# Optimization experiments

Hardware: AMD Instinct MI355X
Metric: run time of the kernel (lower is better)

## Reference

```python
import jax, jax.numpy as jnp
import numpy as np

EPS = 1e-8


def setup_inputs() -> dict:
    key = jax.random.key(0)
    k1, k2, k3 = jax.random.split(key, 3)
    T, B, d, n = 1024, 8, 64, 64
    v = jax.random.normal(k1, (T, B, d), dtype=jnp.float32)
    k = jax.random.normal(k2, (T, B, n), dtype=jnp.float32)
    alpha = jax.random.uniform(k3, (T, B, n), dtype=jnp.float32)
    return {"v": v, "k": k, "alpha": alpha}


def reference(v, k, alpha):
    # v: (T,B,d), k: (T,B,n), alpha: (T,B,n) in [0,1] -> S: (T,B,d,n)
    outer = jnp.einsum('tbd,tbn->tbdn', v, k)          # (T,B,d,n)
    log_alpha = jnp.log(jnp.maximum(alpha, EPS))       # clamp_min(1e-8)
    cumprod = jnp.exp(jnp.cumsum(log_alpha, axis=0))   # (T,B,n)
    decay = cumprod / (cumprod[-1:] + EPS)             # normalize by last step
    weighted = outer * decay[:, :, None, :]            # (T,B,d,n)
    S = jnp.cumsum(weighted, axis=0)
    return S
```

## Files before the change

### kernel.cpp

```cpp
#include <hip/hip_runtime.h>

#define T_DIM 1024
#define B_DIM 8
#define D_DIM 64
#define N_DIM 64

typedef float v4f __attribute__((ext_vector_type(4)));

#define WS_W 0
#define WS_PSUM 524288

template <int C>
__global__ __launch_bounds__(1024) void decay_w_kernel(
    const float* __restrict__ alpha, const float* __restrict__ kk,
    float* __restrict__ ws) {
  constexpr int LEN = T_DIM / C;
  constexpr int CPT = C / 16;
  const int b = blockIdx.x;
  const int tid = threadIdx.x;
  const int n = tid & 63;
  const int ci = tid >> 6;

  __shared__ float ls[C][N_DIM];

#pragma unroll
  for (int cc = 0; cc < CPT; ++cc) {
    const int c = cc * 16 + ci;
    float s = 0.f;
#pragma unroll 8
    for (int i = 0; i < LEN; ++i) {
      const int t = c * LEN + i;
      s += logf(fmaxf(alpha[((size_t)t * B_DIM + b) * N_DIM + n], 1e-8f));
    }
    ls[c][n] = s;
  }
  __syncthreads();

#pragma unroll
  for (int cc = 0; cc < CPT; ++cc) {
    const int c = cc * 16 + ci;
    float pre = 0.f, tot = 0.f;
#pragma unroll
    for (int j = 0; j < C; ++j) {
      const float sv = ls[j][n];
      tot += sv;
      if (j < c) pre += sv;
    }
    const float invden = 1.0f / (expf(tot) + 1e-8f);
    float cum = pre;
#pragma unroll 4
    for (int i = 0; i < LEN; ++i) {
      const size_t idx = ((size_t)(c * LEN + i) * B_DIM + b) * N_DIM + n;
      cum += logf(fmaxf(alpha[idx], 1e-8f));
      ws[WS_W + idx] = kk[idx] * expf(cum) * invden;
    }
  }
}

template <int C>
__global__ __launch_bounds__(256) void chunk_psum_kernel(
    const float* __restrict__ v, float* __restrict__ ws) {
  constexpr int LEN = T_DIM / C;
  const int bid = blockIdx.x;
  const int dt = bid & 3;
  const int b  = (bid >> 2) & 7;
  const int c  = bid >> 5;
  const int tid = threadIdx.x;
  const int d  = dt * 16 + (tid >> 4);
  const int n0 = (tid & 15) * 4;

  const float* __restrict__ vp = v + (size_t)b * D_DIM + d;
  const float* __restrict__ wp = ws + WS_W + (size_t)b * N_DIM + n0;

  v4f acc = {0.f, 0.f, 0.f, 0.f};
#pragma unroll 8
  for (int i = 0; i < LEN; ++i) {
    const int t = c * LEN + i;
    const float vv = vp[(size_t)t * (B_DIM * D_DIM)];
    const v4f w4 = *(const v4f*)(wp + (size_t)t * (B_DIM * N_DIM));
    acc.x = fmaf(vv, w4.x, acc.x);
    acc.y = fmaf(vv, w4.y, acc.y);
    acc.z = fmaf(vv, w4.z, acc.z);
    acc.w = fmaf(vv, w4.w, acc.w);
  }
  *(v4f*)(ws + WS_PSUM + (((size_t)c * B_DIM + b) * D_DIM + d) * N_DIM + n0) = acc;
}

template <int C>
__global__ __launch_bounds__(256) void scan_store_kernel(
    const float* __restrict__ v, const float* __restrict__ ws,
    float* __restrict__ out) {
  constexpr int LEN = T_DIM / C;
  const int bid = blockIdx.x;
  const int dt = bid & 3;
  const int b  = (bid >> 2) & 7;
  const int c  = bid >> 5;
  const int tid = threadIdx.x;
  const int d  = dt * 16 + (tid >> 4);
  const int n0 = (tid & 15) * 4;

  const float* __restrict__ vp = v + (size_t)b * D_DIM + d;
  const float* __restrict__ wp = ws + WS_W + (size_t)b * N_DIM + n0;
  const float* __restrict__ pp = ws + WS_PSUM + ((size_t)b * D_DIM + d) * N_DIM + n0;

  v4f acc = {0.f, 0.f, 0.f, 0.f};
#pragma unroll 4
  for (int j = 0; j < c; ++j) {
    const v4f p = *(const v4f*)(pp + (size_t)j * (B_DIM * D_DIM * N_DIM));
    acc.x += p.x; acc.y += p.y; acc.z += p.z; acc.w += p.w;
  }

#pragma unroll 8
  for (int i = 0; i < LEN; ++i) {
    const int t = c * LEN + i;
    const float vv = vp[(size_t)t * (B_DIM * D_DIM)];
    const v4f w4 = *(const v4f*)(wp + (size_t)t * (B_DIM * N_DIM));
    acc.x = fmaf(vv, w4.x, acc.x);
    acc.y = fmaf(vv, w4.y, acc.y);
    acc.z = fmaf(vv, w4.z, acc.z);
    acc.w = fmaf(vv, w4.w, acc.w);
    __builtin_nontemporal_store(
        acc, (v4f*)(out + (((size_t)t * B_DIM + b) * D_DIM + d) * N_DIM + n0));
  }
}

extern "C" void kernel_launch(void* const* d_in, const int* in_sizes, int n_in,
                              void* d_out, int out_size, void* d_ws, size_t ws_size,
                              hipStream_t stream) {
  const float* v     = (const float*)d_in[0];
  const float* k     = (const float*)d_in[1];
  const float* alpha = (const float*)d_in[2];
  float* out = (float*)d_out;
  float* ws  = (float*)d_ws;

  const size_t needed32 = (size_t)(WS_PSUM + 32 * B_DIM * D_DIM * N_DIM) * sizeof(float);
  if (ws_size >= needed32) {
    decay_w_kernel<32><<<B_DIM, 1024, 0, stream>>>(alpha, k, ws);
    chunk_psum_kernel<32><<<32 * 32, 256, 0, stream>>>(v, ws);
    scan_store_kernel<32><<<32 * 32, 256, 0, stream>>>(v, ws, out);
  } else {
    decay_w_kernel<16><<<B_DIM, 1024, 0, stream>>>(alpha, k, ws);
    chunk_psum_kernel<16><<<16 * 32, 256, 0, stream>>>(v, ws);
    scan_store_kernel<16><<<16 * 32, 256, 0, stream>>>(v, ws, out);
  }
}
```

Measured before the change: 183.1 us.

## Split decay into parallel chunk kernels, add psum prefix kernel, raise chunks to 64

Replaces the single-block-per-batch decay kernel with two kernels over 64 chunks per batch, so the log/exp decay work is spread across 512 blocks instead of 8. Adds a separate prefix-sum kernel over per-chunk partial sums so scan_store reads one precomputed prefix instead of looping over all previous chunks. Raises the chunk count to 64 when the workspace allows, fully unrolls the inner loops, and switches output stores from nontemporal to regular. The cost is two extra launches, more workspace traffic for the prefix buffer, and the risk that regular stores pollute cache.

```diff
diff --git a/kernel.cpp b/kernel.cpp
--- a/kernel.cpp
+++ b/kernel.cpp
@@ -7,53 +7,53 @@
 
 typedef float v4f __attribute__((ext_vector_type(4)));
 
+#define DC_CHUNKS 64
+#define DC_LEN 16
+
+#define SLAB (B_DIM * D_DIM * N_DIM)
+
 #define WS_W 0
-#define WS_PSUM 524288
+#define WS_PSUM (T_DIM * B_DIM * N_DIM)
 
-template <int C>
-__global__ __launch_bounds__(1024) void decay_w_kernel(
+__global__ __launch_bounds__(64) void decay_chunksum_kernel(
+    const float* __restrict__ alpha, float* __restrict__ lsum) {
+  const int b = blockIdx.x >> 6;
+  const int c = blockIdx.x & 63;
+  const int n = threadIdx.x;
+
+  float s = 0.f;
+#pragma unroll
+  for (int i = 0; i < DC_LEN; ++i) {
+    const int t = c * DC_LEN + i;
+    s += logf(fmaxf(alpha[((size_t)t * B_DIM + b) * N_DIM + n], 1e-8f));
+  }
+  lsum[((size_t)b * DC_CHUNKS + c) * N_DIM + n] = s;
+}
+
+__global__ __launch_bounds__(64) void decay_w_kernel(
     const float* __restrict__ alpha, const float* __restrict__ kk,
-    float* __restrict__ ws) {
-  constexpr int LEN = T_DIM / C;
-  constexpr int CPT = C / 16;
-  const int b = blockIdx.x;
-  const int tid = threadIdx.x;
-  const int n = tid & 63;
-  const int ci = tid >> 6;
+    const float* __restrict__ lsum, float* __restrict__ w) {
+  const int b = blockIdx.x >> 6;
+  const int c = blockIdx.x & 63;
+  const int n = threadIdx.x;
 
-  __shared__ float ls[C][N_DIM];
+  const float* __restrict__ lp = lsum + (size_t)b * DC_CHUNKS * N_DIM + n;
+  float pre = 0.f, tot = 0.f;
+#pragma unroll 8
+  for (int j = 0; j < DC_CHUNKS; ++j) {
+    const float sj = lp[(size_t)j * N_DIM];
+    pre += (j < c) ? sj : 0.f;
+    tot += sj;
+  }
+  const float invden = 1.0f / (expf(tot) + 1e-8f);
 
+  float cum = pre;
 #pragma unroll
-  for (int cc = 0; cc < CPT; ++cc) {
-    const int c = cc * 16 + ci;
-    float s = 0.f;
-#pragma unroll 8
-    for (int i = 0; i < LEN; ++i) {
-      const int t = c * LEN + i;
-      s += logf(fmaxf(alpha[((size_t)t * B_DIM + b) * N_DIM + n], 1e-8f));
-    }
-    ls[c][n] = s;
-  }
-  __syncthreads();
-
-#pragma unroll
-  for (int cc = 0; cc < CPT; ++cc) {
-    const int c = cc * 16 + ci;
-    float pre = 0.f, tot = 0.f;
-#pragma unroll
-    for (int j = 0; j < C; ++j) {
-      const float sv = ls[j][n];
-      tot += sv;
-      if (j < c) pre += sv;
-    }
-    const float invden = 1.0f / (expf(tot) + 1e-8f);
-    float cum = pre;
-#pragma unroll 4
-    for (int i = 0; i < LEN; ++i) {
-      const size_t idx = ((size_t)(c * LEN + i) * B_DIM + b) * N_DIM + n;
-      cum += logf(fmaxf(alpha[idx], 1e-8f));
-      ws[WS_W + idx] = kk[idx] * expf(cum) * invden;
-    }
+  for (int i = 0; i < DC_LEN; ++i) {
+    const int t = c * DC_LEN + i;
+    const size_t idx = ((size_t)t * B_DIM + b) * N_DIM + n;
+    cum += logf(fmaxf(alpha[idx], 1e-8f));
+    w[idx] = kk[idx] * expf(cum) * invden;
   }
 }
 
@@ -73,7 +73,7 @@
   const float* __restrict__ wp = ws + WS_W + (size_t)b * N_DIM + n0;
 
   v4f acc = {0.f, 0.f, 0.f, 0.f};
-#pragma unroll 8
+#pragma unroll
   for (int i = 0; i < LEN; ++i) {
     const int t = c * LEN + i;
     const float vv = vp[(size_t)t * (B_DIM * D_DIM)];
@@ -84,6 +84,21 @@
     acc.w = fmaf(vv, w4.w, acc.w);
   }
   *(v4f*)(ws + WS_PSUM + (((size_t)c * B_DIM + b) * D_DIM + d) * N_DIM + n0) = acc;
+}
+
+template <int C>
+__global__ __launch_bounds__(256) void psum_prefix_kernel(float* __restrict__ ws) {
+  const int q = blockIdx.x * 256 + threadIdx.x;
+  v4f* __restrict__ ps  = (v4f*)(ws + WS_PSUM);
+  v4f* __restrict__ pxs = ps + (size_t)C * (SLAB / 4);
+
+  v4f run = {0.f, 0.f, 0.f, 0.f};
+#pragma unroll 8
+  for (int c = 0; c < C; ++c) {
+    const v4f p = ps[(size_t)c * (SLAB / 4) + q];
+    pxs[(size_t)c * (SLAB / 4) + q] = run;
+    run.x += p.x; run.y += p.y; run.z += p.z; run.w += p.w;
+  }
 }
 
 template <int C>
@@ -101,16 +116,12 @@
 
   const float* __restrict__ vp = v + (size_t)b * D_DIM + d;
   const float* __restrict__ wp = ws + WS_W + (size_t)b * N_DIM + n0;
-  const float* __restrict__ pp = ws + WS_PSUM + ((size_t)b * D_DIM + d) * N_DIM + n0;
+  const float* __restrict__ px = ws + WS_PSUM + (size_t)C * SLAB +
+                                 (((size_t)c * B_DIM + b) * D_DIM + d) * N_DIM + n0;
 
-  v4f acc = {0.f, 0.f, 0.f, 0.f};
-#pragma unroll 4
-  for (int j = 0; j < c; ++j) {
-    const v4f p = *(const v4f*)(pp + (size_t)j * (B_DIM * D_DIM * N_DIM));
-    acc.x += p.x; acc.y += p.y; acc.z += p.z; acc.w += p.w;
-  }
+  v4f acc = *(const v4f*)px;
 
-#pragma unroll 8
+#pragma unroll
   for (int i = 0; i < LEN; ++i) {
     const int t = c * LEN + i;
     const float vv = vp[(size_t)t * (B_DIM * D_DIM)];
@@ -119,9 +130,19 @@
     acc.y = fmaf(vv, w4.y, acc.y);
     acc.z = fmaf(vv, w4.z, acc.z);
     acc.w = fmaf(vv, w4.w, acc.w);
-    __builtin_nontemporal_store(
-        acc, (v4f*)(out + (((size_t)t * B_DIM + b) * D_DIM + d) * N_DIM + n0));
+    *(v4f*)(out + (((size_t)t * B_DIM + b) * D_DIM + d) * N_DIM + n0) = acc;
   }
+}
+
+template <int C>
+static void launch_all(const float* v, const float* k, const float* alpha,
+                       float* out, float* ws, hipStream_t stream) {
+  float* lsum = ws + WS_PSUM + (size_t)2 * C * SLAB;
+  decay_chunksum_kernel<<<B_DIM * DC_CHUNKS, 64, 0, stream>>>(alpha, lsum);
+  decay_w_kernel<<<B_DIM * DC_CHUNKS, 64, 0, stream>>>(alpha, k, lsum, ws + WS_W);
+  chunk_psum_kernel<C><<<C * B_DIM * 4, 256, 0, stream>>>(v, ws);
+  psum_prefix_kernel<C><<<SLAB / 4 / 256, 256, 0, stream>>>(ws);
+  scan_store_kernel<C><<<C * B_DIM * 4, 256, 0, stream>>>(v, ws, out);
 }
 
 extern "C" void kernel_launch(void* const* d_in, const int* in_sizes, int n_in,
@@ -133,14 +154,11 @@
   float* out = (float*)d_out;
   float* ws  = (float*)d_ws;
 
-  const size_t needed32 = (size_t)(WS_PSUM + 32 * B_DIM * D_DIM * N_DIM) * sizeof(float);
-  if (ws_size >= needed32) {
-    decay_w_kernel<32><<<B_DIM, 1024, 0, stream>>>(alpha, k, ws);
-    chunk_psum_kernel<32><<<32 * 32, 256, 0, stream>>>(v, ws);
-    scan_store_kernel<32><<<32 * 32, 256, 0, stream>>>(v, ws, out);
+  const size_t need64 =
+      (size_t)(WS_PSUM + 2 * 64 * SLAB + B_DIM * DC_CHUNKS * N_DIM) * sizeof(float);
+  if (ws_size >= need64) {
+    launch_all<64>(v, k, alpha, out, ws, stream);
   } else {
-    decay_w_kernel<16><<<B_DIM, 1024, 0, stream>>>(alpha, k, ws);
-    chunk_psum_kernel<16><<<16 * 32, 256, 0, stream>>>(v, ws);
-    scan_store_kernel<16><<<16 * 32, 256, 0, stream>>>(v, ws, out);
+    launch_all<16>(v, k, alpha, out, ws, stream);
   }
 }
```

Measured after the change: 164.8 us. 1.11x faster.
